# Kernel tuning notes

Measured on AMD Instinct MI355X. Metric: run time of the kernel, lower is better.

Reference implementation:

```python
import jax, jax.numpy as jnp
import numpy as np

EPS = 1e-5  # torch BatchNorm1d default

def _batchnorm(x, gamma, beta):
    # Training-mode BatchNorm1d: biased variance over the batch dim.
    mean = jnp.mean(x, axis=0)
    var = jnp.mean(jnp.square(x - mean), axis=0)
    return (x - mean) * jax.lax.rsqrt(var + EPS) * gamma + beta

def setup_inputs() -> dict:
    key = jax.random.key(0)
    ks = jax.random.split(key, 8)
    N, nfeat, nhid, nclass = 32768, 2048, 4096, 512
    x = jax.random.normal(ks[0], (N, nfeat), dtype=jnp.float32)
    y = jax.random.normal(ks[1], (N, nclass), dtype=jnp.float32)
    # Linear params (kaiming-uniform-ish scale)
    W1 = jax.random.uniform(ks[2], (nhid, nfeat), jnp.float32, -1.0, 1.0) / np.sqrt(nfeat)
    b1 = jax.random.uniform(ks[3], (nhid,), jnp.float32, -1.0, 1.0) / np.sqrt(nfeat)
    W2 = jax.random.uniform(ks[4], (nclass, nhid), jnp.float32, -1.0, 1.0) / np.sqrt(nhid)
    b2 = jax.random.uniform(ks[5], (nclass,), jnp.float32, -1.0, 1.0) / np.sqrt(nhid)
    # BatchNorm affine params (torch init: gamma=1, beta=0)
    bn1_g = jnp.ones((nfeat,), jnp.float32)
    bn1_b = jnp.zeros((nfeat,), jnp.float32)
    bn2_g = jnp.ones((nhid,), jnp.float32)
    bn2_b = jnp.zeros((nhid,), jnp.float32)
    # InteractionUnit: single learnable interaction strength beta
    beta = jnp.array(0.5, jnp.float32)
    return {"x": x, "y": y, "W1": W1, "b1": b1, "W2": W2, "b2": b2,
            "bn1_g": bn1_g, "bn1_b": bn1_b, "bn2_g": bn2_g, "bn2_b": bn2_b,
            "beta": beta}

def reference(x, y, W1, b1, W2, b2, bn1_g, bn1_b, bn2_g, bn2_b, beta):
    h = _batchnorm(x, bn1_g, bn1_b)                 # [N, nfeat]
    h = jax.nn.relu(h @ W1.T + b1)                  # [N, nhid]
    h = _batchnorm(h, bn2_g, bn2_b)                 # [N, nhid]
    out = h @ W2.T + b2 + beta * y                  # [N, nclass]
    return out
```

## Files before the change

### kernel.cpp

```cpp
#include <hip/hip_runtime.h>

typedef __bf16 v8bf __attribute__((ext_vector_type(8)));
typedef float  v16f __attribute__((ext_vector_type(16)));
typedef float  f4   __attribute__((ext_vector_type(4)));
typedef unsigned int uint;
typedef unsigned short ushort;
typedef uint   v4u  __attribute__((ext_vector_type(4)));
typedef uint   v2u  __attribute__((ext_vector_type(2)));

#define GLAS(p) ((const __attribute__((address_space(1))) void*)(p))
#define LDAS(p) ((__attribute__((address_space(3))) void*)(p))

__device__ __forceinline__ ushort f32_to_bf16(float f) {
    uint u = __builtin_bit_cast(uint, f);
    uint r = u + 0x7FFFu + ((u >> 16) & 1u);
    return (ushort)(r >> 16);
}
__device__ __forceinline__ float bflo(uint v) { return __builtin_bit_cast(float, v << 16); }
__device__ __forceinline__ float bfhi(uint v) { return __builtin_bit_cast(float, v & 0xFFFF0000u); }

__global__ void colstats_cvt(const float* __restrict__ x, ushort* __restrict__ xb,
                             float* __restrict__ sum, float* __restrict__ ssum,
                             int ncols, int rows) {
    int c4 = blockIdx.x * blockDim.x + threadIdx.x;
    int q = ncols >> 2;
    size_t base = (size_t)blockIdx.y * rows * q + c4;
    const f4* x4 = (const f4*)x;
    v2u* o = (v2u*)xb;
    f4 s = {0.f, 0.f, 0.f, 0.f}, qq = {0.f, 0.f, 0.f, 0.f};
#pragma unroll 4
    for (int r = 0; r < rows; ++r) {
        f4 v = x4[base + (size_t)r * q];
        s += v; qq += v * v;
        union { ushort us[4]; v2u u; } p;
        p.us[0] = f32_to_bf16(v.x); p.us[1] = f32_to_bf16(v.y);
        p.us[2] = f32_to_bf16(v.z); p.us[3] = f32_to_bf16(v.w);
        o[base + (size_t)r * q] = p.u;
    }
    atomicAdd(&sum[4 * c4 + 0], s.x);  atomicAdd(&ssum[4 * c4 + 0], qq.x);
    atomicAdd(&sum[4 * c4 + 1], s.y);  atomicAdd(&ssum[4 * c4 + 1], qq.y);
    atomicAdd(&sum[4 * c4 + 2], s.z);  atomicAdd(&ssum[4 * c4 + 2], qq.z);
    atomicAdd(&sum[4 * c4 + 3], s.w);  atomicAdd(&ssum[4 * c4 + 3], qq.w);
}

__global__ void colstats_bf16(const ushort* __restrict__ h, float* __restrict__ sum,
                              float* __restrict__ ssum, int ncols, int rows) {
    int cp = blockIdx.x * blockDim.x + threadIdx.x;
    int half = ncols >> 1;
    const uint* h32 = (const uint*)h;
    size_t base = (size_t)blockIdx.y * rows * half + cp;
    float s0 = 0.f, q0 = 0.f, s1 = 0.f, q1 = 0.f;
#pragma unroll 4
    for (int r = 0; r < rows; ++r) {
        uint v = h32[base + (size_t)r * half];
        float a = bflo(v), b = bfhi(v);
        s0 += a; q0 += a * a;
        s1 += b; q1 += b * b;
    }
    atomicAdd(&sum[2 * cp], s0);  atomicAdd(&ssum[2 * cp], q0);
    atomicAdd(&sum[2 * cp + 1], s1); atomicAdd(&ssum[2 * cp + 1], q1);
}

__global__ void bn_finalize(const float* __restrict__ sum, const float* __restrict__ ssum,
                            const float* __restrict__ g, const float* __restrict__ b,
                            float* __restrict__ s, float* __restrict__ t, float invN) {
    int c = blockIdx.x * blockDim.x + threadIdx.x;
    float m = sum[c] * invN;
    float var = fmaxf(ssum[c] * invN - m * m, 0.f);
    float rs = rsqrtf(var + 1e-5f);
    float sc = rs * g[c];
    s[c] = sc;
    t[c] = b[c] - m * sc;
}

__global__ void fold_w(const float* __restrict__ W, const float* __restrict__ bias,
                       const float* __restrict__ s, const float* __restrict__ t,
                       ushort* __restrict__ Wp, float* __restrict__ bp, int K) {
    int j = blockIdx.x, tx = threadIdx.x;
    const f4* row = (const f4*)(W + (size_t)j * K);
    const f4* s4 = (const f4*)s;
    const f4* t4 = (const f4*)t;
    v2u* orow = (v2u*)(Wp + (size_t)j * K);
    float part = 0.f;
    int K4 = K >> 2;
    for (int k = tx; k < K4; k += 256) {
        f4 v = row[k], sv = s4[k], tv = t4[k];
        part += v.x * tv.x + v.y * tv.y + v.z * tv.z + v.w * tv.w;
        union { ushort us[4]; v2u u; } o;
        o.us[0] = f32_to_bf16(v.x * sv.x);
        o.us[1] = f32_to_bf16(v.y * sv.y);
        o.us[2] = f32_to_bf16(v.z * sv.z);
        o.us[3] = f32_to_bf16(v.w * sv.w);
        orow[k] = o.u;
    }
    __shared__ float red[256];
    red[tx] = part;
    __syncthreads();
    for (int off = 128; off > 0; off >>= 1) {
        if (tx < off) red[tx] += red[tx + off];
        __syncthreads();
    }
    if (tx == 0) bp[j] = bias[j] + red[0];
}

template <int EPI>
__global__ __launch_bounds__(256) void gemm_bt(
    const ushort* __restrict__ A, const ushort* __restrict__ B,
    void* __restrict__ Cout, const float* __restrict__ bias,
    const float* __restrict__ Y, const float* __restrict__ betaPtr,
    int M, int Ncol, int K) {
    __shared__ __align__(16) ushort lsA[128 * 64];
    __shared__ __align__(16) ushort lsB[128 * 64];
    const int tid = threadIdx.x;
    const int wave = tid >> 6, lane = tid & 63;
    const int wm = wave >> 1, wn = wave & 1;
    const int l32 = lane & 31, lq = lane >> 5;
    const int m0 = blockIdx.y * 128, n0 = blockIdx.x * 128;

    const int srow = lane >> 3;
    const int sgc  = (lane & 7) ^ (lane >> 3);

    v16f acc[2][2] = {};

    for (int k0 = 0; k0 < K; k0 += 64) {
#pragma unroll
        for (int q = 0; q < 4; ++q) {
            const int g0 = (q * 4 + wave) << 6;
            const int row = (g0 >> 3) + srow;
            const ushort* sa = A + (size_t)(m0 + row) * K + k0 + sgc * 8;
            const ushort* sb = B + (size_t)(n0 + row) * K + k0 + sgc * 8;
            __builtin_amdgcn_global_load_lds(GLAS(sa), LDAS(&lsA[g0 * 8]), 16, 0, 0);
            __builtin_amdgcn_global_load_lds(GLAS(sb), LDAS(&lsB[g0 * 8]), 16, 0, 0);
        }
        __syncthreads();
#pragma unroll
        for (int kk = 0; kk < 64; kk += 16) {
            v8bf a[2], b[2];
            const int cbase = (kk >> 3) + lq;
#pragma unroll
            for (int i = 0; i < 2; ++i) {
                const int ra = wm * 64 + i * 32 + l32;
                const int pa = ra * 8 + (cbase ^ (ra & 7));
                a[i] = __builtin_bit_cast(v8bf, *(const v4u*)&lsA[pa * 8]);
            }
#pragma unroll
            for (int j = 0; j < 2; ++j) {
                const int rb = wn * 64 + j * 32 + l32;
                const int pb = rb * 8 + (cbase ^ (rb & 7));
                b[j] = __builtin_bit_cast(v8bf, *(const v4u*)&lsB[pb * 8]);
            }
#pragma unroll
            for (int i = 0; i < 2; ++i)
#pragma unroll
                for (int j = 0; j < 2; ++j)
                    acc[i][j] = __builtin_amdgcn_mfma_f32_32x32x16_bf16(a[i], b[j], acc[i][j], 0, 0, 0);
        }
        __syncthreads();
    }

    const float betaV = (EPI == 1) ? betaPtr[0] : 0.f;
#pragma unroll
    for (int j = 0; j < 2; ++j) {
        const int col = n0 + wn * 64 + j * 32 + l32;
        const float bj = bias[col];
#pragma unroll
        for (int i = 0; i < 2; ++i) {
#pragma unroll
            for (int reg = 0; reg < 16; ++reg) {
                const int row = m0 + wm * 64 + i * 32 + (reg & 3) + 8 * (reg >> 2) + 4 * lq;
                float v = acc[i][j][reg] + bj;
                if (EPI == 0) {
                    v = v > 0.f ? v : 0.f;
                    ((ushort*)Cout)[(size_t)row * Ncol + col] = f32_to_bf16(v);
                } else {
                    v += betaV * Y[(size_t)row * Ncol + col];
                    ((float*)Cout)[(size_t)row * Ncol + col] = v;
                }
            }
        }
    }
}

extern "C" void kernel_launch(void* const* d_in, const int* in_sizes, int n_in,
                              void* d_out, int out_size, void* d_ws, size_t ws_size,
                              hipStream_t stream) {
    const float* x    = (const float*)d_in[0];
    const float* y    = (const float*)d_in[1];
    const float* W1   = (const float*)d_in[2];
    const float* b1   = (const float*)d_in[3];
    const float* W2   = (const float*)d_in[4];
    const float* b2   = (const float*)d_in[5];
    const float* bn1g = (const float*)d_in[6];
    const float* bn1b = (const float*)d_in[7];
    const float* bn2g = (const float*)d_in[8];
    const float* bn2b = (const float*)d_in[9];
    const float* beta = (const float*)d_in[10];

    constexpr int Nb = 32768, F = 2048, H = 4096, C = 512;

    char* w = (char*)d_ws;
    ushort* xb  = (ushort*)w;
    ushort* h1  = (ushort*)(w + (size_t)Nb * F * 2);
    ushort* w1p = (ushort*)(w + (size_t)Nb * F * 2 + (size_t)Nb * H * 2);
    ushort* w2p = (ushort*)((char*)w1p + (size_t)H * F * 2);
    float*  fb  = (float*)((char*)w2p + (size_t)C * H * 2);
    float* b1p = fb;
    float* b2p = b1p + H;
    float* sum1 = b2p + C;
    float* ss1  = sum1 + F;
    float* s1   = ss1 + F;
    float* t1   = s1 + F;
    float* sum2 = t1 + F;
    float* ss2  = sum2 + H;
    float* s2   = ss2 + H;
    float* t2   = s2 + H;

    hipMemsetAsync(sum1, 0, sizeof(float) * 2 * F, stream);
    hipMemsetAsync(sum2, 0, sizeof(float) * 2 * H, stream);

    colstats_cvt<<<dim3(F / 4 / 256, 256), 256, 0, stream>>>(x, xb, sum1, ss1, F, Nb / 256);
    bn_finalize<<<F / 256, 256, 0, stream>>>(sum1, ss1, bn1g, bn1b, s1, t1, 1.f / Nb);
    fold_w<<<H, 256, 0, stream>>>(W1, b1, s1, t1, w1p, b1p, F);
    gemm_bt<0><<<dim3(H / 128, Nb / 128), 256, 0, stream>>>(xb, w1p, h1, b1p, nullptr, nullptr, Nb, H, F);
    colstats_bf16<<<dim3(H / 2 / 256, 128), 256, 0, stream>>>(h1, sum2, ss2, H, Nb / 128);
    bn_finalize<<<H / 256, 256, 0, stream>>>(sum2, ss2, bn2g, bn2b, s2, t2, 1.f / Nb);
    fold_w<<<C, 256, 0, stream>>>(W2, b2, s2, t2, w2p, b2p, H);
    gemm_bt<1><<<dim3(C / 128, Nb / 128), 256, 0, stream>>>(h1, w2p, d_out, b2p, y, beta, Nb, C, H);
    (void)in_sizes; (void)n_in; (void)out_size; (void)ws_size;
}
```

Measured before the change: 1.399 ms.

## Fuse BN2 column statistics into GEMM1 epilogue and drop atomics for BN1 stats

Column sum and sum-of-squares for the second batchnorm are now accumulated in the first GEMM's epilogue, reduced across waves in LDS, and atomically added per column. This removes the separate pass that re-read the 256MB bf16 hidden activation. BN1 statistics are written as per-block partials into a scratch area (reusing h1) and reduced in a new finalize kernel instead of using float atomics. fold_w now handles one row per wave with shuffle reductions. Statistics are computed from fp32 values before bf16 rounding, so they differ slightly from stats taken on the stored bf16 data.

```diff
diff --git a/kernel.cpp b/kernel.cpp
--- a/kernel.cpp
+++ b/kernel.cpp
@@ -16,12 +16,10 @@
     uint r = u + 0x7FFFu + ((u >> 16) & 1u);
     return (ushort)(r >> 16);
 }
-__device__ __forceinline__ float bflo(uint v) { return __builtin_bit_cast(float, v << 16); }
-__device__ __forceinline__ float bfhi(uint v) { return __builtin_bit_cast(float, v & 0xFFFF0000u); }
-
-__global__ void colstats_cvt(const float* __restrict__ x, ushort* __restrict__ xb,
-                             float* __restrict__ sum, float* __restrict__ ssum,
-                             int ncols, int rows) {
+
+__global__ __launch_bounds__(256) void colstats_cvt(
+    const float* __restrict__ x, ushort* __restrict__ xb,
+    float* __restrict__ ps, float* __restrict__ pq, int ncols, int rows) {
     int c4 = blockIdx.x * blockDim.x + threadIdx.x;
     int q = ncols >> 2;
     size_t base = (size_t)blockIdx.y * rows * q + c4;
@@ -37,28 +35,26 @@
         p.us[2] = f32_to_bf16(v.z); p.us[3] = f32_to_bf16(v.w);
         o[base + (size_t)r * q] = p.u;
     }
-    atomicAdd(&sum[4 * c4 + 0], s.x);  atomicAdd(&ssum[4 * c4 + 0], qq.x);
-    atomicAdd(&sum[4 * c4 + 1], s.y);  atomicAdd(&ssum[4 * c4 + 1], qq.y);
-    atomicAdd(&sum[4 * c4 + 2], s.z);  atomicAdd(&ssum[4 * c4 + 2], qq.z);
-    atomicAdd(&sum[4 * c4 + 3], s.w);  atomicAdd(&ssum[4 * c4 + 3], qq.w);
-}
-
-__global__ void colstats_bf16(const ushort* __restrict__ h, float* __restrict__ sum,
-                              float* __restrict__ ssum, int ncols, int rows) {
-    int cp = blockIdx.x * blockDim.x + threadIdx.x;
-    int half = ncols >> 1;
-    const uint* h32 = (const uint*)h;
-    size_t base = (size_t)blockIdx.y * rows * half + cp;
-    float s0 = 0.f, q0 = 0.f, s1 = 0.f, q1 = 0.f;
-#pragma unroll 4
-    for (int r = 0; r < rows; ++r) {
-        uint v = h32[base + (size_t)r * half];
-        float a = bflo(v), b = bfhi(v);
-        s0 += a; q0 += a * a;
-        s1 += b; q1 += b * b;
-    }
-    atomicAdd(&sum[2 * cp], s0);  atomicAdd(&ssum[2 * cp], q0);
-    atomicAdd(&sum[2 * cp + 1], s1); atomicAdd(&ssum[2 * cp + 1], q1);
+    ((f4*)ps)[(size_t)blockIdx.y * q + c4] = s;
+    ((f4*)pq)[(size_t)blockIdx.y * q + c4] = qq;
+}
+
+__global__ void bn_finalize_part(const float* __restrict__ ps, const float* __restrict__ pq,
+                                 const float* __restrict__ g, const float* __restrict__ b,
+                                 float* __restrict__ s, float* __restrict__ t,
+                                 float invN, int ncols, int nparts) {
+    int c = blockIdx.x * blockDim.x + threadIdx.x;
+    float S = 0.f, Q = 0.f;
+    for (int p = 0; p < nparts; ++p) {
+        S += ps[(size_t)p * ncols + c];
+        Q += pq[(size_t)p * ncols + c];
+    }
+    float m = S * invN;
+    float var = fmaxf(Q * invN - m * m, 0.f);
+    float rs = rsqrtf(var + 1e-5f);
+    float sc = rs * g[c];
+    s[c] = sc;
+    t[c] = b[c] - m * sc;
 }
 
 __global__ void bn_finalize(const float* __restrict__ sum, const float* __restrict__ ssum,
@@ -73,18 +69,20 @@
     t[c] = b[c] - m * sc;
 }
 
-__global__ void fold_w(const float* __restrict__ W, const float* __restrict__ bias,
-                       const float* __restrict__ s, const float* __restrict__ t,
-                       ushort* __restrict__ Wp, float* __restrict__ bp, int K) {
-    int j = blockIdx.x, tx = threadIdx.x;
-    const f4* row = (const f4*)(W + (size_t)j * K);
+__global__ __launch_bounds__(256) void fold_w(
+    const float* __restrict__ W, const float* __restrict__ bias,
+    const float* __restrict__ s, const float* __restrict__ t,
+    ushort* __restrict__ Wp, float* __restrict__ bp, int K) {
+    int row = blockIdx.x * 4 + (threadIdx.x >> 6);
+    int lane = threadIdx.x & 63;
+    const f4* wr = (const f4*)(W + (size_t)row * K);
     const f4* s4 = (const f4*)s;
     const f4* t4 = (const f4*)t;
-    v2u* orow = (v2u*)(Wp + (size_t)j * K);
+    v2u* orow = (v2u*)(Wp + (size_t)row * K);
     float part = 0.f;
     int K4 = K >> 2;
-    for (int k = tx; k < K4; k += 256) {
-        f4 v = row[k], sv = s4[k], tv = t4[k];
+    for (int k = lane; k < K4; k += 64) {
+        f4 v = wr[k], sv = s4[k], tv = t4[k];
         part += v.x * tv.x + v.y * tv.y + v.z * tv.z + v.w * tv.w;
         union { ushort us[4]; v2u u; } o;
         o.us[0] = f32_to_bf16(v.x * sv.x);
@@ -93,14 +91,9 @@
         o.us[3] = f32_to_bf16(v.w * sv.w);
         orow[k] = o.u;
     }
-    __shared__ float red[256];
-    red[tx] = part;
-    __syncthreads();
-    for (int off = 128; off > 0; off >>= 1) {
-        if (tx < off) red[tx] += red[tx + off];
-        __syncthreads();
-    }
-    if (tx == 0) bp[j] = bias[j] + red[0];
+#pragma unroll
+    for (int off = 32; off > 0; off >>= 1) part += __shfl_down(part, off);
+    if (lane == 0) bp[row] = bias[row] + part;
 }
 
 template <int EPI>
@@ -108,6 +101,7 @@
     const ushort* __restrict__ A, const ushort* __restrict__ B,
     void* __restrict__ Cout, const float* __restrict__ bias,
     const float* __restrict__ Y, const float* __restrict__ betaPtr,
+    float* __restrict__ colS, float* __restrict__ colQ,
     int M, int Ncol, int K) {
     __shared__ __align__(16) ushort lsA[128 * 64];
     __shared__ __align__(16) ushort lsB[128 * 64];
@@ -159,6 +153,7 @@
     }
 
     const float betaV = (EPI == 1) ? betaPtr[0] : 0.f;
+    float sj[2] = {0.f, 0.f}, qj[2] = {0.f, 0.f};
 #pragma unroll
     for (int j = 0; j < 2; ++j) {
         const int col = n0 + wn * 64 + j * 32 + l32;
@@ -171,12 +166,32 @@
                 float v = acc[i][j][reg] + bj;
                 if (EPI == 0) {
                     v = v > 0.f ? v : 0.f;
+                    sj[j] += v; qj[j] += v * v;
                     ((ushort*)Cout)[(size_t)row * Ncol + col] = f32_to_bf16(v);
                 } else {
                     v += betaV * Y[(size_t)row * Ncol + col];
                     ((float*)Cout)[(size_t)row * Ncol + col] = v;
                 }
             }
+        }
+    }
+
+    if (EPI == 0) {
+        float* cs = (float*)lsA;
+        float* cq = cs + 512;
+        const int p = wm * 2 + lq;
+#pragma unroll
+        for (int j = 0; j < 2; ++j) {
+            const int ci = wn * 64 + j * 32 + l32;
+            cs[p * 128 + ci] = sj[j];
+            cq[p * 128 + ci] = qj[j];
+        }
+        __syncthreads();
+        if (tid < 128) {
+            float S = cs[tid] + cs[128 + tid] + cs[256 + tid] + cs[384 + tid];
+            float Q = cq[tid] + cq[128 + tid] + cq[256 + tid] + cq[384 + tid];
+            atomicAdd(&colS[n0 + tid], S);
+            atomicAdd(&colQ[n0 + tid], Q);
         }
     }
 }
@@ -197,6 +212,7 @@
     const float* beta = (const float*)d_in[10];
 
     constexpr int Nb = 32768, F = 2048, H = 4096, C = 512;
+    constexpr int NPART = 256;
 
     char* w = (char*)d_ws;
     ushort* xb  = (ushort*)w;
@@ -206,25 +222,25 @@
     float*  fb  = (float*)((char*)w2p + (size_t)C * H * 2);
     float* b1p = fb;
     float* b2p = b1p + H;
-    float* sum1 = b2p + C;
-    float* ss1  = sum1 + F;
-    float* s1   = ss1 + F;
+    float* sum2 = b2p + C;
+    float* ss2  = sum2 + H;
+    float* s1   = ss2 + H;
     float* t1   = s1 + F;
-    float* sum2 = t1 + F;
-    float* ss2  = sum2 + H;
-    float* s2   = ss2 + H;
+    float* s2   = t1 + F;
     float* t2   = s2 + H;
-
-    hipMemsetAsync(sum1, 0, sizeof(float) * 2 * F, stream);
+    float* ps1 = (float*)h1;
+    float* pq1 = ps1 + (size_t)NPART * F;
+
     hipMemsetAsync(sum2, 0, sizeof(float) * 2 * H, stream);
 
-    colstats_cvt<<<dim3(F / 4 / 256, 256), 256, 0, stream>>>(x, xb, sum1, ss1, F, Nb / 256);
-    bn_finalize<<<F / 256, 256, 0, stream>>>(sum1, ss1, bn1g, bn1b, s1, t1, 1.f / Nb);
-    fold_w<<<H, 256, 0, stream>>>(W1, b1, s1, t1, w1p, b1p, F);
-    gemm_bt<0><<<dim3(H / 128, Nb / 128), 256, 0, stream>>>(xb, w1p, h1, b1p, nullptr, nullptr, Nb, H, F);
-    colstats_bf16<<<dim3(H / 2 / 256, 128), 256, 0, stream>>>(h1, sum2, ss2, H, Nb / 128);
+    colstats_cvt<<<dim3(F / 4 / 256, NPART), 256, 0, stream>>>(x, xb, ps1, pq1, F, Nb / NPART);
+    bn_finalize_part<<<F / 256, 256, 0, stream>>>(ps1, pq1, bn1g, bn1b, s1, t1, 1.f / Nb, F, NPART);
+    fold_w<<<H / 4, 256, 0, stream>>>(W1, b1, s1, t1, w1p, b1p, F);
+    gemm_bt<0><<<dim3(H / 128, Nb / 128), 256, 0, stream>>>(
+        xb, w1p, h1, b1p, nullptr, nullptr, sum2, ss2, Nb, H, F);
     bn_finalize<<<H / 256, 256, 0, stream>>>(sum2, ss2, bn2g, bn2b, s2, t2, 1.f / Nb);
-    fold_w<<<C, 256, 0, stream>>>(W2, b2, s2, t2, w2p, b2p, H);
-    gemm_bt<1><<<dim3(C / 128, Nb / 128), 256, 0, stream>>>(h1, w2p, d_out, b2p, y, beta, Nb, C, H);
+    fold_w<<<C / 4, 256, 0, stream>>>(W2, b2, s2, t2, w2p, b2p, H);
+    gemm_bt<1><<<dim3(C / 128, Nb / 128), 256, 0, stream>>>(
+        h1, w2p, d_out, b2p, y, beta, nullptr, nullptr, Nb, C, H);
     (void)in_sizes; (void)n_in; (void)out_size; (void)ws_size;
 }
```

New measurement: 1.553 ms. 1.11x slower.
